# Kernel optimization log

Measured on AMD Instinct MI355X. Metric: run time of the kernel, lower is better.

## Reference

```python
import jax, jax.numpy as jnp
import numpy as np

N = 200000      # total nodes
D = 256         # input_dim
H = 256         # hidden_dim
O = 256         # output_dim
G = 1024        # n_graphs


def setup_inputs() -> dict:
    key = jax.random.key(0)
    ks = jax.random.split(key, 8)
    w = lambda k, shp, fan: jax.random.normal(k, shp, jnp.float32) / np.sqrt(fan)
    # evenly partitioned, sorted segment ids -> every graph non-empty
    batch = ((jnp.arange(N) * G) // N).astype(jnp.int32)
    return {
        "node_features": jax.random.normal(ks[0], (N, D), jnp.float32),
        "batch": batch,
        "num_segments": G,
        "W1": w(ks[1], (D, H), D), "b1": jnp.zeros((H,), jnp.float32),
        "W2": w(ks[2], (H, H), H), "b2": jnp.zeros((H,), jnp.float32),
        "W3": w(ks[3], (H, O), H), "b3": jnp.zeros((O,), jnp.float32),
        "aW1": w(ks[4], (D, H), D), "ab1": jnp.zeros((H,), jnp.float32),
        "aW2": w(ks[5], (H, 1), H), "ab2": jnp.zeros((1,), jnp.float32),
    }


def reference(node_features, batch, num_segments,
              W1, b1, W2, b2, W3, b3, aW1, ab1, aW2, ab2):
    silu = jax.nn.silu
    # MLP: Linear -> SiLU -> Linear -> SiLU -> Linear
    h = silu(node_features @ W1 + b1)
    h = silu(h @ W2 + b2)
    x = h @ W3 + b3                      # (N, O)
    # attention logits: Linear -> SiLU -> Linear(->1)
    logits = (silu(node_features @ aW1 + ab1) @ aW2 + ab2)[:, 0]  # (N,)
    # per-segment stable softmax via segment max/sum
    m = jax.ops.segment_max(logits, batch, num_segments=num_segments)
    ew = jnp.exp(logits - m[batch])
    denom = jax.ops.segment_sum(ew, batch, num_segments=num_segments)
    weights = ew / denom[batch]          # (N,)
    # weighted segment sum -> (G, O)
    out = jax.ops.segment_sum(x * weights[:, None], batch, num_segments=num_segments)
    return out
```

## Files before the change

kernel.cpp:

```cpp
#include <hip/hip_runtime.h>

#define N_NODES 200000
#define DIM 256
#define G_SEG 1024
#define MT 128
#define LDA 264
#define NT 8
#define KSTEPS 8

typedef __bf16 bf16x8 __attribute__((ext_vector_type(8)));
typedef float f32x4 __attribute__((ext_vector_type(4)));
typedef unsigned short us16_t __attribute__((ext_vector_type(16)));
typedef unsigned short us8_t __attribute__((ext_vector_type(8)));
typedef unsigned short us4_t __attribute__((ext_vector_type(4)));

__device__ __forceinline__ unsigned short f2bf(float f) {
  unsigned int u = __float_as_uint(f);
  u = u + 0x7FFFu + ((u >> 16) & 1u);
  return (unsigned short)(u >> 16);
}

__device__ __forceinline__ bf16x8 ld_frag(const unsigned short* p) {
  us8_t r = *(const us8_t*)p;
  return __builtin_bit_cast(bf16x8, r);
}

__device__ __forceinline__ float silu(float v) {
  return v * __builtin_amdgcn_rcpf(1.f + __expf(-v));
}

__device__ __forceinline__ void stage_x(const float* __restrict__ X,
                                        unsigned short* A, int base, int tid) {
  #pragma unroll 4
  for (int i = 0; i < 32; ++i) {
    int flat = i * 256 + tid;
    int row = flat >> 6;
    int c4 = flat & 63;
    int grow = base + row;
    float4 v = make_float4(0.f, 0.f, 0.f, 0.f);
    if (grow < N_NODES) v = *(const float4*)(X + (size_t)grow * DIM + c4 * 4);
    us4_t h;
    h[0] = f2bf(v.x); h[1] = f2bf(v.y); h[2] = f2bf(v.z); h[3] = f2bf(v.w);
    *(us4_t*)(A + row * LDA + c4 * 4) = h;
  }
}

__device__ __forceinline__ void gemm_k256_T(const unsigned short* __restrict__ Wb,
                                            const unsigned short* A,
                                            f32x4 acc[NT][4],
                                            int wcol0, int quad, int l15) {
  for (int ks = 0; ks < KSTEPS; ++ks) {
    int koff = ks * 32 + quad * 8;
    bf16x8 wfr[4];
    #pragma unroll
    for (int u = 0; u < 4; ++u)
      wfr[u] = ld_frag(Wb + (size_t)(wcol0 + u * 16 + l15) * 256 + koff);
    #pragma unroll
    for (int t = 0; t < NT; ++t) {
      bf16x8 xfr = ld_frag(A + (t * 16 + l15) * LDA + koff);
      #pragma unroll
      for (int u = 0; u < 4; ++u)
        acc[t][u] = __builtin_amdgcn_mfma_f32_16x16x32_bf16(wfr[u], xfr, acc[t][u], 0, 0, 0);
    }
  }
}

__device__ __forceinline__ void zero_acc(f32x4 acc[NT][4]) {
  #pragma unroll
  for (int t = 0; t < NT; ++t)
    #pragma unroll
    for (int u = 0; u < 4; ++u)
      acc[t][u] = (f32x4){0.f, 0.f, 0.f, 0.f};
}

__global__ __launch_bounds__(256) void k_prep(
    const float* __restrict__ W1, const float* __restrict__ W2,
    const float* __restrict__ W3, const float* __restrict__ aW1,
    unsigned short* __restrict__ Wb1, unsigned short* __restrict__ Wb2,
    unsigned short* __restrict__ Wb3, unsigned short* __restrict__ aWb1,
    float* __restrict__ out, float* __restrict__ denom) {
  __shared__ float tlds[64][257];
  int b = blockIdx.x, tid = threadIdx.x;
  if (b < 1024) {
    out[b * 256 + tid] = 0.f;
    return;
  }
  if (b == 1024) {
    #pragma unroll
    for (int i = 0; i < 4; ++i) denom[tid * 4 + i] = 0.f;
    return;
  }
  int bb = b - 1025;
  int mat = bb >> 2, kc = bb & 3, k0 = kc * 64;
  const float* W = (mat == 0) ? W1 : (mat == 1) ? W2 : (mat == 2) ? W3 : aW1;
  unsigned short* Wb = (mat == 0) ? Wb1 : (mat == 1) ? Wb2 : (mat == 2) ? Wb3 : aWb1;
  #pragma unroll 8
  for (int i = 0; i < 64; ++i)
    tlds[i][tid] = W[(size_t)(k0 + i) * 256 + tid];
  __syncthreads();
  #pragma unroll
  for (int rep = 0; rep < 4; ++rep) {
    int flat = rep * 256 + tid;
    int n = flat >> 2, c = flat & 3;
    us16_t v;
    #pragma unroll
    for (int j = 0; j < 16; ++j) v[j] = f2bf(tlds[c * 16 + j][n]);
    *(us16_t*)(Wb + (size_t)n * 256 + k0 + c * 16) = v;
  }
}

__global__ __launch_bounds__(256, 2) void k_fused(
    const float* __restrict__ X, const int* __restrict__ batch,
    const unsigned short* __restrict__ aWb1, const float* __restrict__ ab1,
    const float* __restrict__ aW2, const float* __restrict__ ab2,
    const unsigned short* __restrict__ Wb1, const float* __restrict__ b1,
    const unsigned short* __restrict__ Wb2, const float* __restrict__ b2,
    const unsigned short* __restrict__ Wb3, const float* __restrict__ b3,
    float* __restrict__ out, float* __restrict__ denom) {
  __shared__ unsigned short a_lds[MT * LDA];
  __shared__ float l_lds[MT];
  __shared__ float ew0[MT], ew1[MT];
  __shared__ float seg_lds[2];
  int tid = threadIdx.x;
  int base = blockIdx.x * MT;
  stage_x(X, a_lds, base, tid);
  if (tid < MT) l_lds[tid] = 0.f;
  if (tid < 2) seg_lds[tid] = 0.f;
  __syncthreads();

  int wave = tid >> 6, lane = tid & 63, quad = lane >> 4, l15 = lane & 15;
  int wcol0 = wave * 64;
  int fq = wcol0 + quad * 4;
  f32x4 acc[NT][4];

  zero_acc(acc);
  gemm_k256_T(aWb1, a_lds, acc, wcol0, quad, l15);
  {
    float4 ab1c[4], aw2c[4];
    #pragma unroll
    for (int u = 0; u < 4; ++u) {
      ab1c[u] = *(const float4*)(ab1 + fq + u * 16);
      aw2c[u] = *(const float4*)(aW2 + fq + u * 16);
    }
    #pragma unroll
    for (int t = 0; t < NT; ++t) {
      float p = 0.f;
      #pragma unroll
      for (int u = 0; u < 4; ++u) {
        const float* bb = (const float*)&ab1c[u];
        const float* ww = (const float*)&aw2c[u];
        #pragma unroll
        for (int r = 0; r < 4; ++r)
          p += silu(acc[t][u][r] + bb[r]) * ww[r];
      }
      p += __shfl_xor(p, 16); p += __shfl_xor(p, 32);
      if (quad == 0) atomicAdd(&l_lds[t * 16 + l15], p);
    }
  }

  zero_acc(acc);
  gemm_k256_T(Wb1, a_lds, acc, wcol0, quad, l15);
  __syncthreads();
  if (tid < MT) {
    int grow = base + tid;
    float e = 0.f; int ds = 0;
    if (grow < N_NODES) {
      e = __expf(l_lds[tid] + ab2[0]);
      ds = batch[grow] - batch[base];
    }
    ew0[tid] = ds ? 0.f : e;
    ew1[tid] = ds ? e : 0.f;
    if (e != 0.f) atomicAdd(&seg_lds[ds], e);
  }
  {
    float4 bc[4];
    #pragma unroll
    for (int u = 0; u < 4; ++u) bc[u] = *(const float4*)(b1 + fq + u * 16);
    #pragma unroll
    for (int t = 0; t < NT; ++t)
      #pragma unroll
      for (int u = 0; u < 4; ++u) {
        const float* bb = (const float*)&bc[u];
        us4_t h;
        #pragma unroll
        for (int r = 0; r < 4; ++r)
          h[r] = f2bf(silu(acc[t][u][r] + bb[r]));
        *(us4_t*)(a_lds + (t * 16 + l15) * LDA + fq + u * 16) = h;
      }
  }
  __syncthreads();

  zero_acc(acc);
  gemm_k256_T(Wb2, a_lds, acc, wcol0, quad, l15);
  __syncthreads();
  {
    float4 bc[4];
    #pragma unroll
    for (int u = 0; u < 4; ++u) bc[u] = *(const float4*)(b2 + fq + u * 16);
    #pragma unroll
    for (int t = 0; t < NT; ++t)
      #pragma unroll
      for (int u = 0; u < 4; ++u) {
        const float* bb = (const float*)&bc[u];
        us4_t h;
        #pragma unroll
        for (int r = 0; r < 4; ++r)
          h[r] = f2bf(silu(acc[t][u][r] + bb[r]));
        *(us4_t*)(a_lds + (t * 16 + l15) * LDA + fq + u * 16) = h;
      }
  }
  __syncthreads();

  zero_acc(acc);
  gemm_k256_T(Wb3, a_lds, acc, wcol0, quad, l15);
  {
    float4 bc[4];
    #pragma unroll
    for (int u = 0; u < 4; ++u) bc[u] = *(const float4*)(b3 + fq + u * 16);
    float s0a[4][4], s1a[4][4];
    #pragma unroll
    for (int u = 0; u < 4; ++u)
      #pragma unroll
      for (int r = 0; r < 4; ++r) { s0a[u][r] = 0.f; s1a[u][r] = 0.f; }
    #pragma unroll
    for (int t = 0; t < NT; ++t) {
      float w0 = ew0[t * 16 + l15];
      float w1 = ew1[t * 16 + l15];
      #pragma unroll
      for (int u = 0; u < 4; ++u) {
        const float* bb = (const float*)&bc[u];
        #pragma unroll
        for (int r = 0; r < 4; ++r) {
          float x = acc[t][u][r] + bb[r];
          s0a[u][r] += x * w0;
          s1a[u][r] += x * w1;
        }
      }
    }
    int s0 = batch[base];
    #pragma unroll
    for (int u = 0; u < 4; ++u)
      #pragma unroll
      for (int r = 0; r < 4; ++r) {
        float a0 = s0a[u][r];
        a0 += __shfl_xor(a0, 1); a0 += __shfl_xor(a0, 2);
        a0 += __shfl_xor(a0, 4); a0 += __shfl_xor(a0, 8);
        float a1 = s1a[u][r];
        a1 += __shfl_xor(a1, 1); a1 += __shfl_xor(a1, 2);
        a1 += __shfl_xor(a1, 4); a1 += __shfl_xor(a1, 8);
        if (l15 == 0) {
          int col = fq + u * 16 + r;
          atomicAdd(&out[(size_t)s0 * 256 + col], a0);
          if (s0 + 1 < G_SEG && a1 != 0.f)
            atomicAdd(&out[(size_t)(s0 + 1) * 256 + col], a1);
        }
      }
    if (tid < 2) {
      float v = seg_lds[tid];
      if (v != 0.f) atomicAdd(&denom[s0 + tid], v);
    }
  }
}

__global__ __launch_bounds__(256) void k_final(float* __restrict__ out,
                                               const float* __restrict__ denom) {
  int b = blockIdx.x, tid = threadIdx.x;
  float d = denom[b];
  out[b * 256 + tid] *= __builtin_amdgcn_rcpf(d) * (d * __builtin_amdgcn_rcpf(d) > 0.f ? 1.f : 1.f);
}

extern "C" void kernel_launch(void* const* d_in, const int* in_sizes, int n_in,
                              void* d_out, int out_size, void* d_ws, size_t ws_size,
                              hipStream_t stream) {
  const float* X    = (const float*)d_in[0];
  const int* batch  = (const int*)d_in[1];
  const float* W1  = (const float*)d_in[3];
  const float* b1  = (const float*)d_in[4];
  const float* W2  = (const float*)d_in[5];
  const float* b2  = (const float*)d_in[6];
  const float* W3  = (const float*)d_in[7];
  const float* b3  = (const float*)d_in[8];
  const float* aW1 = (const float*)d_in[9];
  const float* ab1 = (const float*)d_in[10];
  const float* aW2 = (const float*)d_in[11];
  const float* ab2 = (const float*)d_in[12];
  float* out = (float*)d_out;

  char* ws = (char*)d_ws;
  unsigned short* Wb1  = (unsigned short*)(ws);
  unsigned short* Wb2  = (unsigned short*)(ws + 131072);
  unsigned short* Wb3  = (unsigned short*)(ws + 262144);
  unsigned short* aWb1 = (unsigned short*)(ws + 393216);
  float* denom = (float*)(ws + 524288);

  hipLaunchKernelGGL(k_prep, dim3(1041), dim3(256), 0, stream,
                     W1, W2, W3, aW1, Wb1, Wb2, Wb3, aWb1, out, denom);
  int nblk = (N_NODES + MT - 1) / MT;
  hipLaunchKernelGGL(k_fused, dim3(nblk), dim3(256), 0, stream,
                     X, batch, aWb1, ab1, aW2, ab2,
                     Wb1, b1, Wb2, b2, Wb3, b3, out, denom);
  hipLaunchKernelGGL(k_final, dim3(G_SEG), dim3(256), 0, stream, out, denom);
}
```

Before: 473.8 us.

## Halve node tile to 64 rows, raise occupancy, simplify addressing and bf16 conversion

Cuts the per-block node tile from 128 to 64 rows, which halves the accumulator registers and LDS per block, and raises launch bounds to 4 blocks per CU. Fragment addresses are precomputed per lane, the k-loop is fully unrolled, and the manual bf16 rounding is replaced by a vector convert. Bounds checks are dropped because 200000 divides evenly by 64. The cost is that weight fragments are reloaded twice as often per node, and there are twice as many global atomics per output column.

Result: slower. 491.0 us (+3.6%).

```diff
diff --git a/kernel.cpp b/kernel.cpp
--- a/kernel.cpp
+++ b/kernel.cpp
@@ -3,12 +3,13 @@
 #define N_NODES 200000
 #define DIM 256
 #define G_SEG 1024
-#define MT 128
+#define MT 64
 #define LDA 264
-#define NT 8
+#define NT 4
 #define KSTEPS 8
 
 typedef __bf16 bf16x8 __attribute__((ext_vector_type(8)));
+typedef __bf16 bf16x4v __attribute__((ext_vector_type(4)));
 typedef float f32x4 __attribute__((ext_vector_type(4)));
 typedef unsigned short us16_t __attribute__((ext_vector_type(16)));
 typedef unsigned short us8_t __attribute__((ext_vector_type(8)));
@@ -29,35 +30,35 @@
   return v * __builtin_amdgcn_rcpf(1.f + __expf(-v));
 }
 
+__device__ __forceinline__ void st_bf4(unsigned short* dst, f32x4 x) {
+  *(bf16x4v*)dst = __builtin_convertvector(x, bf16x4v);
+}
+
 __device__ __forceinline__ void stage_x(const float* __restrict__ X,
                                         unsigned short* A, int base, int tid) {
   #pragma unroll 4
-  for (int i = 0; i < 32; ++i) {
+  for (int i = 0; i < 16; ++i) {
     int flat = i * 256 + tid;
     int row = flat >> 6;
     int c4 = flat & 63;
-    int grow = base + row;
-    float4 v = make_float4(0.f, 0.f, 0.f, 0.f);
-    if (grow < N_NODES) v = *(const float4*)(X + (size_t)grow * DIM + c4 * 4);
-    us4_t h;
-    h[0] = f2bf(v.x); h[1] = f2bf(v.y); h[2] = f2bf(v.z); h[3] = f2bf(v.w);
-    *(us4_t*)(A + row * LDA + c4 * 4) = h;
-  }
-}
-
-__device__ __forceinline__ void gemm_k256_T(const unsigned short* __restrict__ Wb,
-                                            const unsigned short* A,
-                                            f32x4 acc[NT][4],
-                                            int wcol0, int quad, int l15) {
+    float4 v = *(const float4*)(X + (size_t)(base + row) * DIM + c4 * 4);
+    f32x4 f = {v.x, v.y, v.z, v.w};
+    st_bf4(A + row * LDA + c4 * 4, f);
+  }
+}
+
+__device__ __forceinline__ void gemm_k256_T(const unsigned short* __restrict__ wlane,
+                                            const unsigned short* __restrict__ alane,
+                                            f32x4 acc[NT][4]) {
+  #pragma unroll
   for (int ks = 0; ks < KSTEPS; ++ks) {
-    int koff = ks * 32 + quad * 8;
     bf16x8 wfr[4];
     #pragma unroll
     for (int u = 0; u < 4; ++u)
-      wfr[u] = ld_frag(Wb + (size_t)(wcol0 + u * 16 + l15) * 256 + koff);
+      wfr[u] = ld_frag(wlane + u * 16 * 256 + ks * 32);
     #pragma unroll
     for (int t = 0; t < NT; ++t) {
-      bf16x8 xfr = ld_frag(A + (t * 16 + l15) * LDA + koff);
+      bf16x8 xfr = ld_frag(alane + t * 16 * LDA + ks * 32);
       #pragma unroll
       for (int u = 0; u < 4; ++u)
         acc[t][u] = __builtin_amdgcn_mfma_f32_16x16x32_bf16(wfr[u], xfr, acc[t][u], 0, 0, 0);
@@ -109,7 +110,7 @@
   }
 }
 
-__global__ __launch_bounds__(256, 2) void k_fused(
+__global__ __launch_bounds__(256, 4) void k_fused(
     const float* __restrict__ X, const int* __restrict__ batch,
     const unsigned short* __restrict__ aWb1, const float* __restrict__ ab1,
     const float* __restrict__ aW2, const float* __restrict__ ab2,
@@ -131,10 +132,13 @@
   int wave = tid >> 6, lane = tid & 63, quad = lane >> 4, l15 = lane & 15;
   int wcol0 = wave * 64;
   int fq = wcol0 + quad * 4;
+  const unsigned short* alane = a_lds + l15 * LDA + quad * 8;
+  unsigned short* elane = a_lds + l15 * LDA + fq;
+  int woff = (wcol0 + l15) * 256 + quad * 8;
   f32x4 acc[NT][4];
 
   zero_acc(acc);
-  gemm_k256_T(aWb1, a_lds, acc, wcol0, quad, l15);
+  gemm_k256_T(aWb1 + woff, alane, acc);
   {
     float4 ab1c[4], aw2c[4];
     #pragma unroll
@@ -159,18 +163,14 @@
   }
 
   zero_acc(acc);
-  gemm_k256_T(Wb1, a_lds, acc, wcol0, quad, l15);
+  gemm_k256_T(Wb1 + woff, alane, acc);
   __syncthreads();
   if (tid < MT) {
-    int grow = base + tid;
-    float e = 0.f; int ds = 0;
-    if (grow < N_NODES) {
-      e = __expf(l_lds[tid] + ab2[0]);
-      ds = batch[grow] - batch[base];
-    }
+    float e = __expf(l_lds[tid] + ab2[0]);
+    int ds = batch[base + tid] - batch[base];
     ew0[tid] = ds ? 0.f : e;
     ew1[tid] = ds ? e : 0.f;
-    if (e != 0.f) atomicAdd(&seg_lds[ds], e);
+    atomicAdd(&seg_lds[ds], e);
   }
   {
     float4 bc[4];
@@ -181,17 +181,17 @@
       #pragma unroll
       for (int u = 0; u < 4; ++u) {
         const float* bb = (const float*)&bc[u];
-        us4_t h;
+        f32x4 h;
         #pragma unroll
         for (int r = 0; r < 4; ++r)
-          h[r] = f2bf(silu(acc[t][u][r] + bb[r]));
-        *(us4_t*)(a_lds + (t * 16 + l15) * LDA + fq + u * 16) = h;
+          h[r] = silu(acc[t][u][r] + bb[r]);
+        st_bf4(elane + t * 16 * LDA + u * 16, h);
       }
   }
   __syncthreads();
 
   zero_acc(acc);
-  gemm_k256_T(Wb2, a_lds, acc, wcol0, quad, l15);
+  gemm_k256_T(Wb2 + woff, alane, acc);
   __syncthreads();
   {
     float4 bc[4];
@@ -202,17 +202,17 @@
       #pragma unroll
       for (int u = 0; u < 4; ++u) {
         const float* bb = (const float*)&bc[u];
-        us4_t h;
+        f32x4 h;
         #pragma unroll
         for (int r = 0; r < 4; ++r)
-          h[r] = f2bf(silu(acc[t][u][r] + bb[r]));
-        *(us4_t*)(a_lds + (t * 16 + l15) * LDA + fq + u * 16) = h;
+          h[r] = silu(acc[t][u][r] + bb[r]);
+        st_bf4(elane + t * 16 * LDA + u * 16, h);
       }
   }
   __syncthreads();
 
   zero_acc(acc);
-  gemm_k256_T(Wb3, a_lds, acc, wcol0, quad, l15);
+  gemm_k256_T(Wb3 + woff, alane, acc);
   {
     float4 bc[4];
     #pragma unroll
@@ -265,8 +265,7 @@
 __global__ __launch_bounds__(256) void k_final(float* __restrict__ out,
                                                const float* __restrict__ denom) {
   int b = blockIdx.x, tid = threadIdx.x;
-  float d = denom[b];
-  out[b * 256 + tid] *= __builtin_amdgcn_rcpf(d) * (d * __builtin_amdgcn_rcpf(d) > 0.f ? 1.f : 1.f);
+  out[b * 256 + tid] *= __builtin_amdgcn_rcpf(denom[b]);
 }
 
 extern "C" void kernel_launch(void* const* d_in, const int* in_sizes, int n_in,
@@ -295,7 +294,7 @@
 
   hipLaunchKernelGGL(k_prep, dim3(1041), dim3(256), 0, stream,
                      W1, W2, W3, aW1, Wb1, Wb2, Wb3, aWb1, out, denom);
-  int nblk = (N_NODES + MT - 1) / MT;
+  int nblk = N_NODES / MT;
   hipLaunchKernelGGL(k_fused, dim3(nblk), dim3(256), 0, stream,
                      X, batch, aWb1, ab1, aW2, ab2,
                      Wb1, b1, Wb2, b2, Wb3, b3, out, denom);
```
